# Optimization experiments

Measured on AMD Instinct MI355X. Metric: run time of the kernel, lower is better.

The kernel has to match this reference:

```python
import jax, jax.numpy as jnp
import numpy as np

SQRT_2_OVER_PI = 0.7978845608028654  # sqrt(2/pi)

def gelu_tanh(x):
    # F.gelu(x, approximate='tanh')
    return 0.5 * x * (1.0 + jnp.tanh(SQRT_2_OVER_PI * (x + 0.044715 * x * x * x)))

def setup_inputs() -> dict:
    key = jax.random.key(0)
    k1, k2, k3, k4 = jax.random.split(key, 4)
    B, S, DIN, DOUT = 8, 2048, 1152, 4608
    hidden_states = jax.random.normal(k1, (B, S, DIN), dtype=jnp.float32)
    # simulated int8 quantized weights (symmetric, per-output-channel scale)
    w_int8 = jax.random.randint(k2, (DOUT, DIN), -127, 128, dtype=jnp.int32)
    w_scale = jax.random.uniform(k3, (DOUT,), dtype=jnp.float32, minval=0.001, maxval=0.01)
    bias = jax.random.normal(k4, (DOUT,), dtype=jnp.float32) * 0.02
    return {"hidden_states": hidden_states, "w_int8": w_int8, "w_scale": w_scale, "bias": bias}

def reference(hidden_states, w_int8, w_scale, bias):
    # dequantize: per-output-channel scale
    w = w_int8.astype(hidden_states.dtype) * w_scale[:, None]  # [DOUT, DIN]
    # linear projection: [B,S,DIN] @ [DIN,DOUT] -> [B,S,DOUT]
    proj = jnp.einsum('bsd,od->bso', hidden_states, w) + bias
    return gelu_tanh(proj)
```

## Files before the change

kernel.cpp:

```cpp
#include <hip/hip_runtime.h>
#include <cstdint>
#include <cstddef>

#define M_DIM 16384
#define N_DIM 4608
#define K_DIM 1152

typedef __attribute__((ext_vector_type(8))) __bf16 bf16x8;
typedef __attribute__((ext_vector_type(4))) float  f32x4;

__device__ __forceinline__ unsigned short f2bf(float f) {
    unsigned int u = __float_as_uint(f);
    unsigned int r = (u + 0x7FFFu + ((u >> 16) & 1u)) >> 16;
    return (unsigned short)r;
}

__device__ __forceinline__ float gelu_tanh_f(float v) {
    float u = 0.7978845608028654f * (v + 0.044715f * v * v * v);
    float a = fabsf(u);
    float t = __expf(-2.0f * a);
    float th = (1.0f - t) / (1.0f + t);
    th = (u < 0.0f) ? -th : th;
    return 0.5f * v * (1.0f + th);
}


__global__ void cvt_f32_bf16(const float* __restrict__ in,
                             unsigned short* __restrict__ out, int n4) {
    int i = blockIdx.x * 256 + threadIdx.x;
    if (i >= n4) return;
    float4 v = ((const float4*)in)[i];
    ushort4 o;
    o.x = f2bf(v.x); o.y = f2bf(v.y); o.z = f2bf(v.z); o.w = f2bf(v.w);
    ((ushort4*)out)[i] = o;
}

__global__ void cvt_i32_bf16(const int* __restrict__ in,
                             unsigned short* __restrict__ out, int n4) {
    int i = blockIdx.x * 256 + threadIdx.x;
    if (i >= n4) return;
    int4 v = ((const int4*)in)[i];
    ushort4 o;
    o.x = f2bf((float)v.x); o.y = f2bf((float)v.y);
    o.z = f2bf((float)v.z); o.w = f2bf((float)v.w);
    ((ushort4*)out)[i] = o;
}


template <bool PRE>
__global__ void qgelu_gemm(const void* __restrict__ Aptr,
                           const void* __restrict__ Wptr,
                           const float* __restrict__ w_scale,
                           const float* __restrict__ bias,
                           float* __restrict__ out) {
    __shared__ __align__(16) unsigned short As[128 * 64];
    __shared__ __align__(16) unsigned short Bs[128 * 64];

    const int tid    = threadIdx.x;
    const int l      = tid & 63;
    const int wv     = tid >> 6;
    const int lane16 = l & 15;
    const int quad   = l >> 4;
    const int m0 = blockIdx.x * 128;
    const int n0 = blockIdx.y * 128;
    const int wm = (wv & 1) * 64;
    const int wn = (wv >> 1) * 64;

    f32x4 acc[4][4];
#pragma unroll
    for (int i = 0; i < 4; ++i)
#pragma unroll
        for (int j = 0; j < 4; ++j) acc[i][j] = f32x4{0.f, 0.f, 0.f, 0.f};

    const unsigned short* Abf = (const unsigned short*)Aptr;
    const unsigned short* Wbf = (const unsigned short*)Wptr;
    const float* Af = (const float*)Aptr;
    const int*   Wi = (const int*)Wptr;

    for (int kt = 0; kt < K_DIM / 64; ++kt) {
        __syncthreads();
        if constexpr (PRE) {
#pragma unroll
            for (int i = 0; i < 4; ++i) {
                int q   = wv * 64 + i * 256 + l;
                int row = q >> 3;
                int p   = q & 7;
                int c   = p ^ (row & 7);
                const unsigned short* ga =
                    Abf + (size_t)(m0 + row) * K_DIM + kt * 64 + c * 8;
                const unsigned short* gb =
                    Wbf + (size_t)(n0 + row) * K_DIM + kt * 64 + c * 8;
                unsigned short* la = &As[(wv * 64 + i * 256) * 8];
                unsigned short* lb = &Bs[(wv * 64 + i * 256) * 8];
                __builtin_amdgcn_global_load_lds(
                    (const __attribute__((address_space(1))) unsigned int*)ga,
                    (__attribute__((address_space(3))) unsigned int*)la, 16, 0, 0);
                __builtin_amdgcn_global_load_lds(
                    (const __attribute__((address_space(1))) unsigned int*)gb,
                    (__attribute__((address_space(3))) unsigned int*)lb, 16, 0, 0);
            }
        } else {
#pragma unroll
            for (int i = 0; i < 8; ++i) {
                int g    = i * 256 + tid;
                int row  = g >> 4;
                int grp  = g & 15;
                int c    = grp >> 1;
                int half = g & 1;
                int p    = c ^ (row & 7);
                int off  = row * 64 + p * 8 + half * 4;
                {
                    float4 v = *(const float4*)(Af + (size_t)(m0 + row) * K_DIM +
                                                kt * 64 + grp * 4);
                    ushort4 o;
                    o.x = f2bf(v.x); o.y = f2bf(v.y);
                    o.z = f2bf(v.z); o.w = f2bf(v.w);
                    *(ushort4*)(As + off) = o;
                }
                {
                    int4 v = *(const int4*)(Wi + (size_t)(n0 + row) * K_DIM +
                                            kt * 64 + grp * 4);
                    ushort4 o;
                    o.x = f2bf((float)v.x); o.y = f2bf((float)v.y);
                    o.z = f2bf((float)v.z); o.w = f2bf((float)v.w);
                    *(ushort4*)(Bs + off) = o;
                }
            }
        }
        __syncthreads();

#pragma unroll
        for (int s = 0; s < 2; ++s) {
            bf16x8 af[4], bfr[4];
#pragma unroll
            for (int mt = 0; mt < 4; ++mt) {
                int row = wm + mt * 16 + lane16;
                int p   = (s * 4 + quad) ^ (row & 7);
                af[mt]  = *(const bf16x8*)(As + row * 64 + p * 8);
            }
#pragma unroll
            for (int nt = 0; nt < 4; ++nt) {
                int row = wn + nt * 16 + lane16;
                int p   = (s * 4 + quad) ^ (row & 7);
                bfr[nt] = *(const bf16x8*)(Bs + row * 64 + p * 8);
            }
#pragma unroll
            for (int mt = 0; mt < 4; ++mt)
#pragma unroll
                for (int nt = 0; nt < 4; ++nt)
                    acc[mt][nt] = __builtin_amdgcn_mfma_f32_16x16x32_bf16(
                        af[mt], bfr[nt], acc[mt][nt], 0, 0, 0);
        }
    }

#pragma unroll
    for (int nt = 0; nt < 4; ++nt) {
        int n    = n0 + wn + nt * 16 + lane16;
        float sc = w_scale[n];
        float bi = bias[n];
#pragma unroll
        for (int mt = 0; mt < 4; ++mt) {
#pragma unroll
            for (int r = 0; r < 4; ++r) {
                int m   = m0 + wm + mt * 16 + quad * 4 + r;
                float v = acc[mt][nt][r] * sc + bi;
                out[(size_t)m * N_DIM + n] = gelu_tanh_f(v);
            }
        }
    }
}

extern "C" void kernel_launch(void* const* d_in, const int* in_sizes, int n_in,
                              void* d_out, int out_size, void* d_ws, size_t ws_size,
                              hipStream_t stream) {
    const float* hs   = (const float*)d_in[0];
    const int*   w8   = (const int*)d_in[1];
    const float* wsc  = (const float*)d_in[2];
    const float* bias = (const float*)d_in[3];
    float* out = (float*)d_out;

    const size_t nA = (size_t)M_DIM * K_DIM;
    const size_t nW = (size_t)N_DIM * K_DIM;
    const size_t need = (nA + nW) * sizeof(unsigned short);

    dim3 grid(M_DIM / 128, N_DIM / 128);

    if (ws_size >= need) {
        unsigned short* Abf = (unsigned short*)d_ws;
        unsigned short* Wbf = Abf + nA;
        int a4 = (int)(nA / 4), w4 = (int)(nW / 4);
        cvt_f32_bf16<<<(a4 + 255) / 256, 256, 0, stream>>>(hs, Abf, a4);
        cvt_i32_bf16<<<(w4 + 255) / 256, 256, 0, stream>>>(w8, Wbf, w4);
        qgelu_gemm<true><<<grid, 256, 0, stream>>>(Abf, Wbf, wsc, bias, out);
    } else {
        qgelu_gemm<false><<<grid, 256, 0, stream>>>(hs, w8, wsc, bias, out);
    }
}
```

Before: 536.7 us.

## Switch GEMM to int8 MFMA with per-row activation quantization

Replaces the bf16 pre-conversion path with a per-row dynamic int8 quantization of activations and an int8 repack of the weights. The main GEMM then uses i8 MFMA with K tiles of 128 and applies the row and channel scales in the epilogue. This aims to halve operand bytes and K-loop iterations and to use the higher int8 matrix throughput. The trade-off is lower precision on the activations compared with bf16, which may affect accuracy tolerance.

```diff
diff --git a/kernel.cpp b/kernel.cpp
--- a/kernel.cpp
+++ b/kernel.cpp
@@ -8,6 +8,7 @@
 
 typedef __attribute__((ext_vector_type(8))) __bf16 bf16x8;
 typedef __attribute__((ext_vector_type(4))) float  f32x4;
+typedef __attribute__((ext_vector_type(4))) int    v4i;
 
 __device__ __forceinline__ unsigned short f2bf(float f) {
     unsigned int u = __float_as_uint(f);
@@ -24,37 +25,54 @@
     return 0.5f * v * (1.0f + th);
 }
 
-
-__global__ void cvt_f32_bf16(const float* __restrict__ in,
-                             unsigned short* __restrict__ out, int n4) {
+__global__ void quant_rows(const float* __restrict__ A,
+                           signed char* __restrict__ qa,
+                           float* __restrict__ sA) {
+    const int lane = threadIdx.x & 63;
+    const int row  = blockIdx.x * 4 + (threadIdx.x >> 6);
+    const float2* src = (const float2*)(A + (size_t)row * K_DIM);
+    float2 v[9];
+    float amax = 0.f;
+#pragma unroll
+    for (int j = 0; j < 9; ++j) {
+        v[j] = src[j * 64 + lane];
+        amax = fmaxf(amax, fmaxf(fabsf(v[j].x), fabsf(v[j].y)));
+    }
+#pragma unroll
+    for (int off = 32; off > 0; off >>= 1)
+        amax = fmaxf(amax, __shfl_xor(amax, off));
+    amax = fmaxf(amax, 1e-30f);
+    float inv = 127.0f / amax;
+    if (lane == 0) sA[row] = amax * (1.0f / 127.0f);
+    char2* dst = (char2*)(qa + (size_t)row * K_DIM);
+#pragma unroll
+    for (int j = 0; j < 9; ++j) {
+        char2 o;
+        o.x = (signed char)__float2int_rn(v[j].x * inv);
+        o.y = (signed char)__float2int_rn(v[j].y * inv);
+        dst[j * 64 + lane] = o;
+    }
+}
+
+__global__ void pack_w(const int* __restrict__ w,
+                       signed char* __restrict__ qw, int n4) {
     int i = blockIdx.x * 256 + threadIdx.x;
     if (i >= n4) return;
-    float4 v = ((const float4*)in)[i];
-    ushort4 o;
-    o.x = f2bf(v.x); o.y = f2bf(v.y); o.z = f2bf(v.z); o.w = f2bf(v.w);
-    ((ushort4*)out)[i] = o;
-}
-
-__global__ void cvt_i32_bf16(const int* __restrict__ in,
-                             unsigned short* __restrict__ out, int n4) {
-    int i = blockIdx.x * 256 + threadIdx.x;
-    if (i >= n4) return;
-    int4 v = ((const int4*)in)[i];
-    ushort4 o;
-    o.x = f2bf((float)v.x); o.y = f2bf((float)v.y);
-    o.z = f2bf((float)v.z); o.w = f2bf((float)v.w);
-    ((ushort4*)out)[i] = o;
-}
-
-
-template <bool PRE>
-__global__ void qgelu_gemm(const void* __restrict__ Aptr,
-                           const void* __restrict__ Wptr,
-                           const float* __restrict__ w_scale,
-                           const float* __restrict__ bias,
-                           float* __restrict__ out) {
-    __shared__ __align__(16) unsigned short As[128 * 64];
-    __shared__ __align__(16) unsigned short Bs[128 * 64];
+    int4 v = ((const int4*)w)[i];
+    char4 o;
+    o.x = (signed char)v.x; o.y = (signed char)v.y;
+    o.z = (signed char)v.z; o.w = (signed char)v.w;
+    ((char4*)qw)[i] = o;
+}
+
+__global__ void qgelu_gemm_i8(const signed char* __restrict__ Aq,
+                              const signed char* __restrict__ Wq,
+                              const float* __restrict__ sA,
+                              const float* __restrict__ w_scale,
+                              const float* __restrict__ bias,
+                              float* __restrict__ out) {
+    __shared__ __align__(16) signed char As[128 * 128];
+    __shared__ __align__(16) signed char Bs[128 * 128];
 
     const int tid    = threadIdx.x;
     const int l      = tid & 63;
@@ -66,65 +84,121 @@
     const int wm = (wv & 1) * 64;
     const int wn = (wv >> 1) * 64;
 
+    v4i acc[4][4];
+#pragma unroll
+    for (int i = 0; i < 4; ++i)
+#pragma unroll
+        for (int j = 0; j < 4; ++j) acc[i][j] = v4i{0, 0, 0, 0};
+
+    for (int kt = 0; kt < K_DIM / 128; ++kt) {
+        __syncthreads();
+#pragma unroll
+        for (int i = 0; i < 4; ++i) {
+            int q   = wv * 64 + i * 256 + l;
+            int row = q >> 3;
+            int p   = q & 7;
+            int c   = p ^ (row & 7);
+            const signed char* ga = Aq + (size_t)(m0 + row) * K_DIM + kt * 128 + c * 16;
+            const signed char* gb = Wq + (size_t)(n0 + row) * K_DIM + kt * 128 + c * 16;
+            signed char* la = As + (size_t)(wv * 64 + i * 256) * 16;
+            signed char* lb = Bs + (size_t)(wv * 64 + i * 256) * 16;
+            __builtin_amdgcn_global_load_lds(
+                (const __attribute__((address_space(1))) unsigned int*)ga,
+                (__attribute__((address_space(3))) unsigned int*)la, 16, 0, 0);
+            __builtin_amdgcn_global_load_lds(
+                (const __attribute__((address_space(1))) unsigned int*)gb,
+                (__attribute__((address_space(3))) unsigned int*)lb, 16, 0, 0);
+        }
+        __syncthreads();
+
+#pragma unroll
+        for (int s = 0; s < 2; ++s) {
+            v4i af[4], bfr[4];
+#pragma unroll
+            for (int mt = 0; mt < 4; ++mt) {
+                int row = wm + mt * 16 + lane16;
+                int p   = (s * 4 + quad) ^ (row & 7);
+                af[mt]  = *(const v4i*)(As + row * 128 + p * 16);
+            }
+#pragma unroll
+            for (int nt = 0; nt < 4; ++nt) {
+                int row = wn + nt * 16 + lane16;
+                int p   = (s * 4 + quad) ^ (row & 7);
+                bfr[nt] = *(const v4i*)(Bs + row * 128 + p * 16);
+            }
+#pragma unroll
+            for (int mt = 0; mt < 4; ++mt)
+#pragma unroll
+                for (int nt = 0; nt < 4; ++nt)
+                    acc[mt][nt] = __builtin_amdgcn_mfma_i32_16x16x64_i8(
+                        af[mt], bfr[nt], acc[mt][nt], 0, 0, 0);
+        }
+    }
+
+#pragma unroll
+    for (int nt = 0; nt < 4; ++nt) {
+        int n    = n0 + wn + nt * 16 + lane16;
+        float sc = w_scale[n];
+        float bi = bias[n];
+#pragma unroll
+        for (int mt = 0; mt < 4; ++mt) {
+            int mbase = m0 + wm + mt * 16 + quad * 4;
+#pragma unroll
+            for (int r = 0; r < 4; ++r) {
+                float v = (float)acc[mt][nt][r] * sA[mbase + r] * sc + bi;
+                out[(size_t)(mbase + r) * N_DIM + n] = gelu_tanh_f(v);
+            }
+        }
+    }
+}
+
+__global__ void qgelu_gemm_bf16_fused(const float* __restrict__ Af,
+                                      const int* __restrict__ Wi,
+                                      const float* __restrict__ w_scale,
+                                      const float* __restrict__ bias,
+                                      float* __restrict__ out) {
+    __shared__ __align__(16) unsigned short As[128 * 64];
+    __shared__ __align__(16) unsigned short Bs[128 * 64];
+
+    const int tid    = threadIdx.x;
+    const int l      = tid & 63;
+    const int wv     = tid >> 6;
+    const int lane16 = l & 15;
+    const int quad   = l >> 4;
+    const int m0 = blockIdx.x * 128;
+    const int n0 = blockIdx.y * 128;
+    const int wm = (wv & 1) * 64;
+    const int wn = (wv >> 1) * 64;
+
     f32x4 acc[4][4];
 #pragma unroll
     for (int i = 0; i < 4; ++i)
 #pragma unroll
         for (int j = 0; j < 4; ++j) acc[i][j] = f32x4{0.f, 0.f, 0.f, 0.f};
 
-    const unsigned short* Abf = (const unsigned short*)Aptr;
-    const unsigned short* Wbf = (const unsigned short*)Wptr;
-    const float* Af = (const float*)Aptr;
-    const int*   Wi = (const int*)Wptr;
-
     for (int kt = 0; kt < K_DIM / 64; ++kt) {
         __syncthreads();
-        if constexpr (PRE) {
-#pragma unroll
-            for (int i = 0; i < 4; ++i) {
-                int q   = wv * 64 + i * 256 + l;
-                int row = q >> 3;
-                int p   = q & 7;
-                int c   = p ^ (row & 7);
-                const unsigned short* ga =
-                    Abf + (size_t)(m0 + row) * K_DIM + kt * 64 + c * 8;
-                const unsigned short* gb =
-                    Wbf + (size_t)(n0 + row) * K_DIM + kt * 64 + c * 8;
-                unsigned short* la = &As[(wv * 64 + i * 256) * 8];
-                unsigned short* lb = &Bs[(wv * 64 + i * 256) * 8];
-                __builtin_amdgcn_global_load_lds(
-                    (const __attribute__((address_space(1))) unsigned int*)ga,
-                    (__attribute__((address_space(3))) unsigned int*)la, 16, 0, 0);
-                __builtin_amdgcn_global_load_lds(
-                    (const __attribute__((address_space(1))) unsigned int*)gb,
-                    (__attribute__((address_space(3))) unsigned int*)lb, 16, 0, 0);
-            }
-        } else {
-#pragma unroll
-            for (int i = 0; i < 8; ++i) {
-                int g    = i * 256 + tid;
-                int row  = g >> 4;
-                int grp  = g & 15;
-                int c    = grp >> 1;
-                int half = g & 1;
-                int p    = c ^ (row & 7);
-                int off  = row * 64 + p * 8 + half * 4;
-                {
-                    float4 v = *(const float4*)(Af + (size_t)(m0 + row) * K_DIM +
-                                                kt * 64 + grp * 4);
-                    ushort4 o;
-                    o.x = f2bf(v.x); o.y = f2bf(v.y);
-                    o.z = f2bf(v.z); o.w = f2bf(v.w);
-                    *(ushort4*)(As + off) = o;
-                }
-                {
-                    int4 v = *(const int4*)(Wi + (size_t)(n0 + row) * K_DIM +
-                                            kt * 64 + grp * 4);
-                    ushort4 o;
-                    o.x = f2bf((float)v.x); o.y = f2bf((float)v.y);
-                    o.z = f2bf((float)v.z); o.w = f2bf((float)v.w);
-                    *(ushort4*)(Bs + off) = o;
-                }
+#pragma unroll
+        for (int i = 0; i < 8; ++i) {
+            int g    = i * 256 + tid;
+            int row  = g >> 4;
+            int grp  = g & 15;
+            int c    = grp >> 1;
+            int half = g & 1;
+            int p    = c ^ (row & 7);
+            int off  = row * 64 + p * 8 + half * 4;
+            {
+                float4 v = *(const float4*)(Af + (size_t)(m0 + row) * K_DIM + kt * 64 + grp * 4);
+                ushort4 o;
+                o.x = f2bf(v.x); o.y = f2bf(v.y); o.z = f2bf(v.z); o.w = f2bf(v.w);
+                *(ushort4*)(As + off) = o;
+            }
+            {
+                int4 v = *(const int4*)(Wi + (size_t)(n0 + row) * K_DIM + kt * 64 + grp * 4);
+                ushort4 o;
+                o.x = f2bf((float)v.x); o.y = f2bf((float)v.y);
+                o.z = f2bf((float)v.z); o.w = f2bf((float)v.w);
+                *(ushort4*)(Bs + off) = o;
             }
         }
         __syncthreads();
@@ -181,18 +255,19 @@
 
     const size_t nA = (size_t)M_DIM * K_DIM;
     const size_t nW = (size_t)N_DIM * K_DIM;
-    const size_t need = (nA + nW) * sizeof(unsigned short);
+    const size_t need = nA + nW + (size_t)M_DIM * sizeof(float);
 
     dim3 grid(M_DIM / 128, N_DIM / 128);
 
     if (ws_size >= need) {
-        unsigned short* Abf = (unsigned short*)d_ws;
-        unsigned short* Wbf = Abf + nA;
-        int a4 = (int)(nA / 4), w4 = (int)(nW / 4);
-        cvt_f32_bf16<<<(a4 + 255) / 256, 256, 0, stream>>>(hs, Abf, a4);
-        cvt_i32_bf16<<<(w4 + 255) / 256, 256, 0, stream>>>(w8, Wbf, w4);
-        qgelu_gemm<true><<<grid, 256, 0, stream>>>(Abf, Wbf, wsc, bias, out);
+        signed char* qa = (signed char*)d_ws;
+        signed char* qw = qa + nA;
+        float* sA = (float*)(qa + nA + nW);
+        quant_rows<<<M_DIM / 4, 256, 0, stream>>>(hs, qa, sA);
+        int w4 = (int)(nW / 4);
+        pack_w<<<(w4 + 255) / 256, 256, 0, stream>>>(w8, qw, w4);
+        qgelu_gemm_i8<<<grid, 256, 0, stream>>>(qa, qw, sA, wsc, bias, out);
     } else {
-        qgelu_gemm<false><<<grid, 256, 0, stream>>>(hs, w8, wsc, bias, out);
-    }
-}
+        qgelu_gemm_bf16_fused<<<grid, 256, 0, stream>>>(hs, w8, wsc, bias, out);
+    }
+}
```

New measurement: 509.4 us. -5.1%, faster.
